# Performance work log

Hardware: AMD Instinct MI355X
Metric: run time of the kernel (lower is better)

Reference implementation:

```python
import jax, jax.numpy as jnp
import numpy as np

DIM = 1024
N_HEADS = 16
N_KV_HEADS = 4
HEAD_DIM = 64
BATCH = 1
SEQ = 4096
ROPE_BASE = 1000.0


def _rope_tables(seq_len, head_dim, base):
    theta = 1.0 / base ** (jnp.arange(0, head_dim, 2, dtype=jnp.float32) / head_dim)
    freqs = jnp.outer(jnp.arange(seq_len, dtype=jnp.float32), theta)  # [S, hd/2]
    return jnp.cos(freqs), jnp.sin(freqs)


def _apply_rope(x, cos, sin):
    # x: [B, S, H, hd]; cos/sin: [S, hd/2] -> broadcast [1, S, 1, hd/2]
    c = cos[None, :, None, :]
    s = sin[None, :, None, :]
    x1, x2 = x[..., ::2], x[..., 1::2]
    even = x1 * c - x2 * s
    odd = x1 * s + x2 * c
    return jnp.stack([even, odd], axis=-1).reshape(x.shape)


def setup_inputs() -> dict:
    key = jax.random.key(0)
    kx, kq, kk, kv, ko = jax.random.split(key, 5)
    x = jax.random.normal(kx, (BATCH, SEQ, DIM), dtype=jnp.float32)
    # causal mask (1 = attend, 0 = masked)
    mask = jnp.tril(jnp.ones((SEQ, SEQ), dtype=jnp.int32))[None, None, :, :]
    scale = DIM ** -0.5
    Wq = jax.random.normal(kq, (DIM, N_HEADS * HEAD_DIM), dtype=jnp.float32) * scale
    Wk = jax.random.normal(kk, (DIM, N_KV_HEADS * HEAD_DIM), dtype=jnp.float32) * scale
    Wv = jax.random.normal(kv, (DIM, N_KV_HEADS * HEAD_DIM), dtype=jnp.float32) * scale
    Wo = jax.random.normal(ko, (N_HEADS * HEAD_DIM, DIM), dtype=jnp.float32) * scale
    return {"x": x, "mask": mask, "Wq": Wq, "Wk": Wk, "Wv": Wv, "Wo": Wo}


def reference(x, mask, Wq, Wk, Wv, Wo):
    batch, seq_len, _ = x.shape
    q = (x @ Wq).reshape(batch, seq_len, N_HEADS, HEAD_DIM)
    k = (x @ Wk).reshape(batch, seq_len, N_KV_HEADS, HEAD_DIM)
    v = (x @ Wv).reshape(batch, seq_len, N_KV_HEADS, HEAD_DIM)
    cos, sin = _rope_tables(seq_len, HEAD_DIM, ROPE_BASE)
    q = _apply_rope(q, cos, sin)
    k = _apply_rope(k, cos, sin)
    rep = N_HEADS // N_KV_HEADS
    k = jnp.repeat(k, rep, axis=2)  # [B, S, H, hd]
    v = jnp.repeat(v, rep, axis=2)
    q = q.transpose(0, 2, 1, 3)  # [B, H, S, hd]
    k = k.transpose(0, 2, 1, 3)
    v = v.transpose(0, 2, 1, 3)
    scale = HEAD_DIM ** -0.5
    scores = jnp.einsum('bhqd,bhkd->bhqk', q, k) * scale  # [B, H, S, S]
    scores = jnp.where(mask == 0, -jnp.inf, scores)
    attn = jax.nn.softmax(scores, axis=-1)
    out = jnp.einsum('bhqk,bhkd->bhqd', attn, v)
    out = out.transpose(0, 2, 1, 3).reshape(batch, seq_len, N_HEADS * HEAD_DIM)
    return out @ Wo
```

## Files before the change

kernel.cpp:

```cpp
#include <hip/hip_runtime.h>
#include <hip/hip_bf16.h>

typedef __attribute__((ext_vector_type(8))) short short8;
typedef __attribute__((ext_vector_type(4))) float f32x4;
typedef unsigned short u16;
typedef unsigned int u32;

#define SEQ 4096

__device__ __forceinline__ u16 f2bf(float f) {
  return __builtin_bit_cast(u16, __float2bfloat16(f));
}

#if __has_builtin(__builtin_amdgcn_exp2f)
#define EXP2(x) __builtin_amdgcn_exp2f(x)
#else
#define EXP2(x) exp2f(x)
#endif

__device__ __forceinline__ u32 pk2(float a, float b) {
  u32 ua = __builtin_bit_cast(u32, a) + 0x8000u;
  u32 ub = __builtin_bit_cast(u32, b) + 0x8000u;
  return __builtin_amdgcn_perm(ub, ua, 0x07060302);
}

typedef __attribute__((address_space(1))) u32 gas_u32;
typedef __attribute__((address_space(3))) u32 las_u32;
__device__ __forceinline__ void gload16(const u16* g, const u16* l) {
  __builtin_amdgcn_global_load_lds((gas_u32*)(unsigned long long)(const void*)g,
                                   (las_u32*)(u32)(unsigned long long)(const void*)l,
                                   16, 0, 0);
}

__global__ __launch_bounds__(256) void k_prep(const float* __restrict__ x,
                                              u16* __restrict__ xb,
                                              float* __restrict__ cosT,
                                              float* __restrict__ sinT) {
  int bid = blockIdx.x;
  if (bid < 4096) {
    int i = bid * 256 + threadIdx.x;
    float4 v = ((const float4*)x)[i];
    u32 lo = (u32)f2bf(v.x) | ((u32)f2bf(v.y) << 16);
    u32 hi = (u32)f2bf(v.z) | ((u32)f2bf(v.w) << 16);
    uint2 o; o.x = lo; o.y = hi;
    ((uint2*)xb)[i] = o;
  } else {
    int tid = (bid - 4096) * 256 + threadIdx.x;
    int pos = tid >> 5, j = tid & 31;
    float theta = exp2f(-0.311430758895f * (float)j);
    float a = (float)pos * theta;
    float s, c;
    sincosf(a, &s, &c);
    cosT[tid] = c;
    sinT[tid] = s;
  }
}

__global__ __launch_bounds__(256) void k_tconvW(const float* __restrict__ Wq,
                                                const float* __restrict__ Wk,
                                                const float* __restrict__ Wv,
                                                const float* __restrict__ Wo,
                                                u16* __restrict__ Wt,
                                                u16* __restrict__ Wto) {
  __shared__ float tile[64][65];
  int bid = blockIdx.x;
  const float* src; u16* dst; int sstride, bx, by;
  if (bid < 256)      { src = Wq; dst = Wt;              sstride = 1024; bx = bid & 15;        by = bid >> 4; }
  else if (bid < 320) { src = Wk; dst = Wt + 1024 * 1024; sstride = 256;  bx = (bid - 256) & 3; by = (bid - 256) >> 2; }
  else if (bid < 384) { src = Wv; dst = Wt + 1280 * 1024; sstride = 256;  bx = (bid - 320) & 3; by = (bid - 320) >> 2; }
  else                { src = Wo; dst = Wto;             sstride = 1024; bx = (bid - 384) & 15; by = (bid - 384) >> 4; }
  const int dstride = 1024;
  int br = by * 64, bc = bx * 64;
  int t = threadIdx.x;
#pragma unroll
  for (int i = 0; i < 16; ++i) {
    int idx = t + i * 256;
    int r = idx >> 6, c = idx & 63;
    tile[r][c] = src[(long)(br + r) * sstride + bc + c];
  }
  __syncthreads();
#pragma unroll
  for (int i = 0; i < 16; ++i) {
    int idx = t + i * 256;
    int cc = idx >> 6, rr = idx & 63;
    dst[(long)(bc + cc) * dstride + br + rr] = f2bf(tile[rr][cc]);
  }
}

__global__ __launch_bounds__(256) void k_gemm(const u16* __restrict__ A,
                                              const u16* __restrict__ Bt,
                                              float* __restrict__ C,
                                              int M, int N, int K) {
  __shared__ __align__(16) u16 a_lds[128 * 64];
  __shared__ __align__(16) u16 b_lds[64 * 64];
  const int bm = blockIdx.x * 128, bn = blockIdx.y * 64;
  const int t = threadIdx.x;
  const int l = t & 63, w = t >> 6;
  const int wm = (w >> 1) * 64, wn = (w & 1) * 32;
  const int lg = l >> 4, ll = l & 15;

  const f32x4 vzero = {0.f, 0.f, 0.f, 0.f};
  f32x4 acc[4][2];
#pragma unroll
  for (int i = 0; i < 4; ++i)
#pragma unroll
    for (int j = 0; j < 2; ++j) acc[i][j] = vzero;

  const u16* ga = A + (long)(bm + w * 32 + (l >> 3)) * K + (l & 7) * 8;
  const u16* gb = Bt + (long)(bn + w * 16 + (l >> 3)) * K + (l & 7) * 8;
  u16* la = a_lds + w * 32 * 64;
  u16* lb = b_lds + w * 16 * 64;
  const long rstep = (long)8 * K;

  for (int kt = 0; kt < K; kt += 64) {
    __syncthreads();
#pragma unroll
    for (int i = 0; i < 4; ++i) gload16(ga + i * rstep, la + i * 512);
#pragma unroll
    for (int i = 0; i < 2; ++i) gload16(gb + i * rstep, lb + i * 512);
    ga += 64; gb += 64;
    __syncthreads();
#pragma unroll
    for (int kc = 0; kc < 2; ++kc) {
      short8 af[4], bfr[2];
#pragma unroll
      for (int mi = 0; mi < 4; ++mi)
        af[mi] = *(const short8*)(a_lds + (wm + mi * 16 + ll) * 64 + kc * 32 + lg * 8);
#pragma unroll
      for (int nb = 0; nb < 2; ++nb)
        bfr[nb] = *(const short8*)(b_lds + (wn + nb * 16 + ll) * 64 + kc * 32 + lg * 8);
#pragma unroll
      for (int mi = 0; mi < 4; ++mi)
#pragma unroll
        for (int nb = 0; nb < 2; ++nb)
          acc[mi][nb] = __builtin_amdgcn_mfma_f32_16x16x32_bf16(af[mi], bfr[nb],
                                                                acc[mi][nb], 0, 0, 0);
    }
  }
  const int rbase = bm + wm + lg * 4;
  const int cbase = bn + wn + ll;
#pragma unroll
  for (int mi = 0; mi < 4; ++mi)
#pragma unroll
    for (int nb = 0; nb < 2; ++nb)
#pragma unroll
      for (int r = 0; r < 4; ++r)
        C[(long)(rbase + mi * 16 + r) * N + cbase + nb * 16] = acc[mi][nb][r];
}

__global__ __launch_bounds__(256) void k_gemmqkv(const u16* __restrict__ A,
                                                 const u16* __restrict__ Bt,
                                                 const float* __restrict__ cosT,
                                                 const float* __restrict__ sinT,
                                                 u16* __restrict__ qb,
                                                 u16* __restrict__ kb,
                                                 u16* __restrict__ vb) {
  const int K = 1024;
  __shared__ __align__(16) u16 a_lds[128 * 64];
  __shared__ __align__(16) u16 b_lds[64 * 64];
  const int bm = blockIdx.x * 128, bn = blockIdx.y * 64;
  const int t = threadIdx.x;
  const int l = t & 63, w = t >> 6;
  const int wm = (w >> 1) * 64, wn = (w & 1) * 32;
  const int lg = l >> 4, ll = l & 15;

  const f32x4 vzero = {0.f, 0.f, 0.f, 0.f};
  f32x4 acc[4][2];
#pragma unroll
  for (int i = 0; i < 4; ++i)
#pragma unroll
    for (int j = 0; j < 2; ++j) acc[i][j] = vzero;

  const u16* ga = A + (long)(bm + w * 32 + (l >> 3)) * K + (l & 7) * 8;
  const u16* gb = Bt + (long)(bn + w * 16 + (l >> 3)) * K + (l & 7) * 8;
  u16* la = a_lds + w * 32 * 64;
  u16* lb = b_lds + w * 16 * 64;
  const long rstep = (long)8 * K;

  for (int kt = 0; kt < K; kt += 64) {
    __syncthreads();
#pragma unroll
    for (int i = 0; i < 4; ++i) gload16(ga + i * rstep, la + i * 512);
#pragma unroll
    for (int i = 0; i < 2; ++i) gload16(gb + i * rstep, lb + i * 512);
    ga += 64; gb += 64;
    __syncthreads();
#pragma unroll
    for (int kc = 0; kc < 2; ++kc) {
      short8 af[4], bfr[2];
#pragma unroll
      for (int mi = 0; mi < 4; ++mi)
        af[mi] = *(const short8*)(a_lds + (wm + mi * 16 + ll) * 64 + kc * 32 + lg * 8);
#pragma unroll
      for (int nb = 0; nb < 2; ++nb)
        bfr[nb] = *(const short8*)(b_lds + (wn + nb * 16 + ll) * 64 + kc * 32 + lg * 8);
#pragma unroll
      for (int mi = 0; mi < 4; ++mi)
#pragma unroll
        for (int nb = 0; nb < 2; ++nb)
          acc[mi][nb] = __builtin_amdgcn_mfma_f32_16x16x32_bf16(af[mi], bfr[nb],
                                                                acc[mi][nb], 0, 0, 0);
    }
  }

  const int rbase = bm + wm + lg * 4;
  const int cbase = bn + wn + ll;
  const int by = blockIdx.y;

  if (by < 20) {
    const float scale = (by < 16) ? 0.18033688011112042f : 1.0f;
#pragma unroll
    for (int mi = 0; mi < 4; ++mi)
#pragma unroll
      for (int nb = 0; nb < 2; ++nb) {
        int col = cbase + nb * 16;
        int j = (col & 63) >> 1;
        long hb = (by < 16) ? (long)(col >> 6) * SEQ
                            : (long)((col - 1024) >> 6) * SEQ;
        u16* dst0 = ((by < 16) ? qb : kb) + (hb) * 64 + (col & 63);
#pragma unroll
        for (int r = 0; r < 4; ++r) {
          float v0 = acc[mi][nb][r];
          float vp = __shfl_xor(v0, 1);
          int row = rbase + mi * 16 + r;
          float c = cosT[(row << 5) + j], s = sinT[(row << 5) + j];
          float res = (ll & 1) ? (vp * s + v0 * c) * scale
                               : (v0 * c - vp * s) * scale;
          dst0[(long)row * 64] = f2bf(res);
        }
      }
  } else {
#pragma unroll
    for (int mi = 0; mi < 4; ++mi)
#pragma unroll
      for (int nb = 0; nb < 2; ++nb) {
        int col = cbase + nb * 16;
        int vd = col - 1280;
        int row0 = rbase + mi * 16;
        uint2 gg;
        gg.x = pk2(acc[mi][nb][0], acc[mi][nb][1]);
        gg.y = pk2(acc[mi][nb][2], acc[mi][nb][3]);
        *(uint2*)(vb + (long)vd * SEQ + row0) = gg;
      }
  }
}

__global__ __launch_bounds__(256) void k_attn(const u16* __restrict__ q,
                                              const u16* __restrict__ kk,
                                              const u16* __restrict__ vT,
                                              u16* __restrict__ o) {
  const int b = blockIdx.x;
  const int h = b & 15;
  const int qt = 63 - (b >> 4);
  const int hkv = h >> 2;
  __shared__ __align__(16) u16 kbuf[2][64 * 64];
  __shared__ __align__(16) u16 vbuf[2][64 * 64];
  __shared__ __align__(16) u16 p_lds[4][16 * 64];
  const int t = threadIdx.x, w = t >> 6, l = t & 63;
  const int lg = l >> 4, ll = l & 15;
  const int grow = w * 16 + ll;
  const f32x4 vzero = {0.f, 0.f, 0.f, 0.f};

  const int lr = l >> 3, lc = l & 7;
  const int cswz = lc ^ (lr & 7);
  const u16* kbase = kk + (long)hkv * SEQ * 64;
  const u16* vbase = vT + (long)hkv * 64 * SEQ;
  const u16* kcur  = kbase + (long)(w * 16 + lr) * 64 + cswz * 8;
  const u16* vcurA = vbase + (long)(w * 16 + lr) * SEQ + cswz * 8;
  const u16* vcurB = vcurA + (long)8 * SEQ;

  u16* pw = p_lds[w];
  const int g0 = (lg ^ (ll & 7)) << 4;
  const int g1 = ((lg ^ (ll & 7)) ^ 4) << 4;
  const int rbyte = ll * 128;
  const char* pwb = (const char*)pw + rbyte;
  const int pwoff = rbyte + (lg & 1) * 8 + (((lg >> 1) ^ (ll & 7)) << 4);

#define ISSUE(BUF)                                                           \
  {                                                                          \
    u16* kld = kbuf[BUF] + w * 1024;                                         \
    u16* vld = vbuf[BUF] + w * 1024;                                         \
    gload16(kcur, kld);          gload16(kcur + 512, kld + 512);             \
    gload16(vcurA, vld);         gload16(vcurB, vld + 512);                  \
    kcur += 4096; vcurA += 64; vcurB += 64;                                  \
  }

  ISSUE(0);
  int buf = 0;

  const int q0 = qt * 64 + w * 16;
  short8 qa0 = *(const short8*)(q + ((long)(h * SEQ + q0 + ll) * 64 + lg * 8));
  short8 qa1 = *(const short8*)(q + ((long)(h * SEQ + q0 + ll) * 64 + 32 + lg * 8));

  f32x4 Oacc[4] = {vzero, vzero, vzero, vzero};
  float lrun = 0.f;

  for (int kt = 0; kt <= qt; ++kt) {
    __syncthreads();
    if (kt < qt) { ISSUE(buf ^ 1); }

    const char* kb_ = (const char*)kbuf[buf] + rbyte;
    const char* vb_ = (const char*)vbuf[buf] + rbyte;
    f32x4 S[4];
    __builtin_amdgcn_s_setprio(1);
#pragma unroll
    for (int st = 0; st < 4; ++st) {
      short8 ka0 = *(const short8*)(kb_ + st * 2048 + g0);
      short8 ka1 = *(const short8*)(kb_ + st * 2048 + g1);
      f32x4 z = vzero;
      z = __builtin_amdgcn_mfma_f32_16x16x32_bf16(ka0, qa0, z, 0, 0, 0);
      z = __builtin_amdgcn_mfma_f32_16x16x32_bf16(ka1, qa1, z, 0, 0, 0);
      S[st] = z;
    }
    __builtin_amdgcn_s_setprio(0);

    if (kt == qt) {
#pragma unroll
      for (int st = 0; st < 4; ++st)
#pragma unroll
        for (int r = 0; r < 4; ++r)
          if (st * 16 + lg * 4 + r > grow) S[st][r] = -__builtin_inff();
    }

    float sl = 0.f;
#pragma unroll
    for (int st = 0; st < 4; ++st) {
      float p0 = EXP2(S[st][0]), p1 = EXP2(S[st][1]);
      float p2 = EXP2(S[st][2]), p3 = EXP2(S[st][3]);
      sl += (p0 + p1) + (p2 + p3);
      uint2 gg;
      gg.x = pk2(p0, p1);
      gg.y = pk2(p2, p3);
      *(uint2*)((char*)pw + (pwoff ^ (st << 5))) = gg;
    }
    lrun += sl;

    asm volatile("" ::: "memory");
    __builtin_amdgcn_s_setprio(1);
#pragma unroll
    for (int kc = 0; kc < 2; ++kc) {
      short8 pa = *(const short8*)(pwb + (kc ? g1 : g0));
#pragma unroll
      for (int nb = 0; nb < 4; ++nb) {
        short8 vv = *(const short8*)(vb_ + nb * 2048 + (kc ? g1 : g0));
        Oacc[nb] = __builtin_amdgcn_mfma_f32_16x16x32_bf16(pa, vv, Oacc[nb],
                                                           0, 0, 0);
      }
    }
    __builtin_amdgcn_s_setprio(0);
    buf ^= 1;
  }
#undef ISSUE

  lrun += __shfl_xor(lrun, 16);
  lrun += __shfl_xor(lrun, 32);

  float i0 = 1.f / __shfl(lrun, (l & 48) | (lg * 4 + 0));
  float i1 = 1.f / __shfl(lrun, (l & 48) | (lg * 4 + 1));
  float i2 = 1.f / __shfl(lrun, (l & 48) | (lg * 4 + 2));
  float i3 = 1.f / __shfl(lrun, (l & 48) | (lg * 4 + 3));
#pragma unroll
  for (int nb = 0; nb < 4; ++nb) {
    int col = h * 64 + nb * 16 + ll;
    o[(long)(q0 + lg * 4 + 0) * 1024 + col] = f2bf(Oacc[nb][0] * i0);
    o[(long)(q0 + lg * 4 + 1) * 1024 + col] = f2bf(Oacc[nb][1] * i1);
    o[(long)(q0 + lg * 4 + 2) * 1024 + col] = f2bf(Oacc[nb][2] * i2);
    o[(long)(q0 + lg * 4 + 3) * 1024 + col] = f2bf(Oacc[nb][3] * i3);
  }
}

extern "C" void kernel_launch(void* const* d_in, const int* in_sizes, int n_in,
                              void* d_out, int out_size, void* d_ws, size_t ws_size,
                              hipStream_t stream) {
  const float* x  = (const float*)d_in[0];
  const float* Wq = (const float*)d_in[2];
  const float* Wk = (const float*)d_in[3];
  const float* Wv = (const float*)d_in[4];
  const float* Wo = (const float*)d_in[5];
  float* out = (float*)d_out;

  char* ws = (char*)d_ws;
  u16* xb    = (u16*)(ws + 25165824);
  u16* Wt    = (u16*)(ws + 33554432);
  u16* Wto   = (u16*)(ws + 36700160);
  u16* qb    = (u16*)(ws + 38797312);
  u16* kb    = (u16*)(ws + 47185920);
  u16* vb    = (u16*)(ws + 49283072);
  float* cosT = (float*)(ws + 51380224);
  float* sinT = (float*)(ws + 51904512);

  k_prep<<<4608, 256, 0, stream>>>(x, xb, cosT, sinT);
  k_tconvW<<<640, 256, 0, stream>>>(Wq, Wk, Wv, Wo, Wt, Wto);

  k_gemmqkv<<<dim3(32, 24), 256, 0, stream>>>(xb, Wt, cosT, sinT, qb, kb, vb);

  k_attn<<<1024, 256, 0, stream>>>(qb, kb, vb, xb);

  k_gemm<<<dim3(32, 16), 256, 0, stream>>>(xb, Wto, out, 4096, 1024, 1024);
}
```

Baseline: 125.4 us.

## Keep softmax probabilities in registers by permuting V storage order

The V projection epilogue now writes V^T with a permuted key order inside each 64-key tile. That order matches the register layout of the S accumulator from the QK^T MFMA, so P can be packed straight into bf16 MFMA operands. This removes the per-wave P scratch buffer in LDS, its writes and reads, and the barrier-like ordering around it. The risk is that the permutation must match exactly between the producer kernel and the attention kernel's V loads, or results will be wrong.

Result: faster. 112.4 us (-10.4%).

```diff
diff --git a/kernel.cpp b/kernel.cpp
--- a/kernel.cpp
+++ b/kernel.cpp
@@ -237,10 +237,13 @@
         int col = cbase + nb * 16;
         int vd = col - 1280;
         int row0 = rbase + mi * 16;
+        int T = row0 & ~63;
+        int kb64 = row0 & 63;
+        int s0 = (kb64 & 32) + ((kb64 & 12) << 1) + ((kb64 & 16) >> 2);
         uint2 gg;
         gg.x = pk2(acc[mi][nb][0], acc[mi][nb][1]);
         gg.y = pk2(acc[mi][nb][2], acc[mi][nb][3]);
-        *(uint2*)(vb + (long)vd * SEQ + row0) = gg;
+        *(uint2*)(vb + (long)vd * SEQ + T + s0) = gg;
       }
   }
 }
@@ -255,7 +258,6 @@
   const int hkv = h >> 2;
   __shared__ __align__(16) u16 kbuf[2][64 * 64];
   __shared__ __align__(16) u16 vbuf[2][64 * 64];
-  __shared__ __align__(16) u16 p_lds[4][16 * 64];
   const int t = threadIdx.x, w = t >> 6, l = t & 63;
   const int lg = l >> 4, ll = l & 15;
   const int grow = w * 16 + ll;
@@ -269,12 +271,9 @@
   const u16* vcurA = vbase + (long)(w * 16 + lr) * SEQ + cswz * 8;
   const u16* vcurB = vcurA + (long)8 * SEQ;
 
-  u16* pw = p_lds[w];
   const int g0 = (lg ^ (ll & 7)) << 4;
   const int g1 = ((lg ^ (ll & 7)) ^ 4) << 4;
   const int rbyte = ll * 128;
-  const char* pwb = (const char*)pw + rbyte;
-  const int pwoff = rbyte + (lg & 1) * 8 + (((lg >> 1) ^ (ll & 7)) << 4);
 
 #define ISSUE(BUF)                                                           \
   {                                                                          \
@@ -322,30 +321,34 @@
           if (st * 16 + lg * 4 + r > grow) S[st][r] = -__builtin_inff();
     }
 
+    float p[4][4];
     float sl = 0.f;
 #pragma unroll
     for (int st = 0; st < 4; ++st) {
-      float p0 = EXP2(S[st][0]), p1 = EXP2(S[st][1]);
-      float p2 = EXP2(S[st][2]), p3 = EXP2(S[st][3]);
-      sl += (p0 + p1) + (p2 + p3);
-      uint2 gg;
-      gg.x = pk2(p0, p1);
-      gg.y = pk2(p2, p3);
-      *(uint2*)((char*)pw + (pwoff ^ (st << 5))) = gg;
+      p[st][0] = EXP2(S[st][0]); p[st][1] = EXP2(S[st][1]);
+      p[st][2] = EXP2(S[st][2]); p[st][3] = EXP2(S[st][3]);
+      sl += (p[st][0] + p[st][1]) + (p[st][2] + p[st][3]);
     }
     lrun += sl;
 
-    asm volatile("" ::: "memory");
+    uint4 u0, u1;
+    u0.x = pk2(p[0][0], p[0][1]); u0.y = pk2(p[0][2], p[0][3]);
+    u0.z = pk2(p[1][0], p[1][1]); u0.w = pk2(p[1][2], p[1][3]);
+    u1.x = pk2(p[2][0], p[2][1]); u1.y = pk2(p[2][2], p[2][3]);
+    u1.z = pk2(p[3][0], p[3][1]); u1.w = pk2(p[3][2], p[3][3]);
+    short8 pa0 = __builtin_bit_cast(short8, u0);
+    short8 pa1 = __builtin_bit_cast(short8, u1);
+
     __builtin_amdgcn_s_setprio(1);
 #pragma unroll
-    for (int kc = 0; kc < 2; ++kc) {
-      short8 pa = *(const short8*)(pwb + (kc ? g1 : g0));
-#pragma unroll
-      for (int nb = 0; nb < 4; ++nb) {
-        short8 vv = *(const short8*)(vb_ + nb * 2048 + (kc ? g1 : g0));
-        Oacc[nb] = __builtin_amdgcn_mfma_f32_16x16x32_bf16(pa, vv, Oacc[nb],
-                                                           0, 0, 0);
-      }
+    for (int nb = 0; nb < 4; ++nb) {
+      short8 vv0 = *(const short8*)(vb_ + nb * 2048 + g0);
+      Oacc[nb] = __builtin_amdgcn_mfma_f32_16x16x32_bf16(pa0, vv0, Oacc[nb], 0, 0, 0);
+    }
+#pragma unroll
+    for (int nb = 0; nb < 4; ++nb) {
+      short8 vv1 = *(const short8*)(vb_ + nb * 2048 + g1);
+      Oacc[nb] = __builtin_amdgcn_mfma_f32_16x16x32_bf16(pa1, vv1, Oacc[nb], 0, 0, 0);
     }
     __builtin_amdgcn_s_setprio(0);
     buf ^= 1;
```
